# Kernel optimization log

Measured on AMD Instinct MI355X. Metric: run time of the kernel, lower is better.

## Reference

```python
import jax, jax.numpy as jnp
import numpy as np

H = 256


def _lstm_cell(inp, hx, cx, Wih, Whh, bih, bhh):
    # PyTorch LSTMCell: gate order i, f, g, o
    gates = inp @ Wih.T + bih + hx @ Whh.T + bhh
    i, f, g, o = jnp.split(gates, 4, axis=-1)
    c = jax.nn.sigmoid(f) * cx + jax.nn.sigmoid(i) * jnp.tanh(g)
    h = jax.nn.sigmoid(o) * jnp.tanh(c)
    return h, c


def _match(p_enc, q_enc, wq, wp, whr_w, whr_b, w_vec, w_b0, Wih, Whh, bih, bhh, reverse):
    # p_enc: (P,B,H) time-major passage; q_enc, wq: (Q,B,H); wp: (P,B,H)
    B = p_enc.shape[1]

    def step(carry, xs):
        hx, cx = carry
        wphp, p_t = xs                                  # (B,H), (B,H)
        wrhr = hx @ whr_w.T + whr_b                     # (B,H)
        g = jnp.tanh(wq + (wphp + wrhr))                # (Q,B,H)
        scores = jnp.einsum('qbh,h->bq', g, w_vec) + w_b0
        alpha = jax.nn.softmax(scores, axis=-1)         # (B,Q)
        attn = jnp.einsum('bq,qbh->bh', alpha, q_enc)   # (B,H)
        inp = jnp.concatenate([p_t, attn], axis=-1)     # (B,2H)
        hx, cx = _lstm_cell(inp, hx, cx, Wih, Whh, bih, bhh)
        return (hx, cx), hx

    init = (jnp.zeros((B, H), p_enc.dtype), jnp.zeros((B, H), p_enc.dtype))
    _, hs = jax.lax.scan(step, init, (wp, p_enc), reverse=reverse)
    return hs  # (P,B,H), always in natural time order


def setup_inputs() -> dict:
    key = jax.random.key(0)
    ks = jax.random.split(key, 20)
    s = 0.05
    return {
        'passage': jax.random.normal(ks[0], (64, 512, H), jnp.float32),
        'question': jax.random.normal(ks[1], (64, 64, H), jnp.float32),
        'whq_w': jax.random.normal(ks[2], (H, H), jnp.float32) * s,
        'whq_b': jax.random.normal(ks[3], (H,), jnp.float32) * s,
        'whp_w': jax.random.normal(ks[4], (H, H), jnp.float32) * s,
        'whp_b': jax.random.normal(ks[5], (H,), jnp.float32) * s,
        'whr_w': jax.random.normal(ks[6], (H, H), jnp.float32) * s,
        'whr_b': jax.random.normal(ks[7], (H,), jnp.float32) * s,
        'w_w': jax.random.normal(ks[8], (1, H), jnp.float32) * s,
        'w_b': jax.random.normal(ks[9], (1,), jnp.float32) * s,
        'fw_Wih': jax.random.normal(ks[10], (4 * H, 2 * H), jnp.float32) * s,
        'fw_Whh': jax.random.normal(ks[11], (4 * H, H), jnp.float32) * s,
        'fw_bih': jax.random.normal(ks[12], (4 * H,), jnp.float32) * s,
        'fw_bhh': jax.random.normal(ks[13], (4 * H,), jnp.float32) * s,
        'bw_Wih': jax.random.normal(ks[14], (4 * H, 2 * H), jnp.float32) * s,
        'bw_Whh': jax.random.normal(ks[15], (4 * H, H), jnp.float32) * s,
        'bw_bih': jax.random.normal(ks[16], (4 * H,), jnp.float32) * s,
        'bw_bhh': jax.random.normal(ks[17], (4 * H,), jnp.float32) * s,
    }


def reference(passage, question, whq_w, whq_b, whp_w, whp_b, whr_w, whr_b,
              w_w, w_b, fw_Wih, fw_Whh, fw_bih, fw_bhh,
              bw_Wih, bw_Whh, bw_bih, bw_bhh):
    p = jnp.swapaxes(passage, 0, 1)    # (P,B,H)
    q = jnp.swapaxes(question, 0, 1)   # (Q,B,H)
    wq = q @ whq_w.T + whq_b           # (Q,B,H)  (dropout p=0.0 -> identity)
    wp = p @ whp_w.T + whp_b           # (P,B,H)
    fw = _match(p, q, wq, wp, whr_w, whr_b, w_w[0], w_b[0],
                fw_Wih, fw_Whh, fw_bih, fw_bhh, reverse=False)
    bw = _match(p, q, wq, wp, whr_w, whr_b, w_w[0], w_b[0],
                bw_Wih, bw_Whh, bw_bih, bw_bhh, reverse=True)
    return jnp.concatenate([fw, bw], axis=-1)  # (P,B,2H)
```

## Files before the change

kernel.cpp:

```cpp
#include <hip/hip_runtime.h>

#define HN 256
#define QN 64
#define PN 512
#define CH 8

typedef float f4 __attribute__((ext_vector_type(4)));

__device__ __forceinline__ float dot4(f4 a, f4 b) {
  return a.x * b.x + a.y * b.y + a.z * b.z + a.w * b.w;
}
__device__ __forceinline__ float fast_sig(float x) {
  return __builtin_amdgcn_rcpf(1.f + __builtin_amdgcn_exp2f(-1.44269504f * x));
}
__device__ __forceinline__ float fast_tanh(float x) {
  return 1.f - 2.f * __builtin_amdgcn_rcpf(1.f + __builtin_amdgcn_exp2f(2.88539008f * x));
}

struct SMem {
  union {
    float q32[QN][HN];
    struct {
      alignas(16) float pgc[CH][1024];
      alignas(16) float wpc[CH][HN];
      alignas(16) float pch[CH][HN];
    } c;
  } u;
  alignas(16) float wqt[QN][HN + 4];
  alignas(16) float ww[HN];
  alignas(16) float hx[HN];
  float cx[HN];
  alignas(16) float wA[HN];
  float wrb[HN];
  float gates[1024];
  float scores[QN];
  alignas(16) float al[QN];
};
static_assert(sizeof(SMem) <= 160 * 1024, "LDS overflow");
static_assert(sizeof(SMem) > 80 * 1024, "want exactly 1 block/CU");

__global__ void __launch_bounds__(1024, 4)
match_kernel(const float* __restrict__ passage, const float* __restrict__ question,
             const float* __restrict__ whq_w, const float* __restrict__ whq_b,
             const float* __restrict__ whp_w, const float* __restrict__ whp_b,
             const float* __restrict__ whr_w, const float* __restrict__ whr_b,
             const float* __restrict__ w_w,
             const float* __restrict__ Wih_f, const float* __restrict__ Whh_f,
             const float* __restrict__ bih_f, const float* __restrict__ bhh_f,
             const float* __restrict__ Wih_b, const float* __restrict__ Whh_b,
             const float* __restrict__ bih_b, const float* __restrict__ bhh_b,
             float* __restrict__ out)
{
  __shared__ SMem sm;
  const int t = threadIdx.x;
  const int bid = blockIdx.x;
  const int e = bid & 7;
  const int dir = e >> 2;
  const int b = ((bid >> 3) << 2) | (e & 3);

  const float* Wih = dir ? Wih_b : Wih_f;
  const float* Whh = dir ? Whh_b : Whh_f;
  const float* bih = dir ? bih_b : bih_f;
  const float* bhh = dir ? bhh_b : bhh_f;

  const int qB = t >> 4;
  const int sg = t & 15;
  const int g2 = t >> 4;

  {
    const int q = t >> 4, c0 = (t & 15) * 16;
    const float* src = question + ((size_t)b * QN + q) * HN + c0;
    #pragma unroll
    for (int m = 0; m < 4; ++m)
      *(f4*)&sm.u.q32[q][c0 + 4 * m] = *(const f4*)(src + 4 * m);
  }
  if (t < HN) {
    sm.hx[t] = 0.f; sm.cx[t] = 0.f;
    sm.wrb[t] = whr_b[t]; sm.ww[t] = w_w[t];
  }
  __syncthreads();

  {
    const int h = t & 255, qh = (t >> 8) * 16;
    float acc[16];
    const float qb = whq_b[h];
    #pragma unroll
    for (int i2 = 0; i2 < 16; ++i2) acc[i2] = qb;
    const float* wrow = whq_w + (size_t)h * HN;
    for (int k = 0; k < HN; k += 4) {
      f4 w4 = *(const f4*)(wrow + k);
      #pragma unroll
      for (int i2 = 0; i2 < 16; ++i2) {
        f4 qv = *(const f4*)&sm.u.q32[qh + i2][k];
        acc[i2] += dot4(w4, qv);
      }
    }
    #pragma unroll
    for (int i2 = 0; i2 < 16; ++i2) sm.wqt[qh + i2][h] = acc[i2];
  }

  float gq[QN];
  #pragma unroll
  for (int q = 0; q < QN; ++q) gq[q] = 0.f;
  {
    const float* wrow = Wih + (size_t)t * 512 + 256;
    for (int i = 0; i < 64; ++i) {
      f4 w = *(const f4*)(wrow + 4 * i);
      #pragma unroll
      for (int q = 0; q < QN; ++q)
        gq[q] += dot4(w, *(const f4*)&sm.u.q32[q][4 * i]);
    }
  }
  const float biasr = bih[t] + bhh[t];
  __syncthreads();

  const int tb = dir ? (PN - 1) : 0;
  const int ts = dir ? -1 : 1;

  for (int s = 0; s < PN; ++s) {
    const int tau = s & (CH - 1);
    if (tau == 0) {
      if (t < 512) {
        const int tt = t >> 6, cc = (t & 63) * 4;
        const int trow = tb + ts * (s + tt);
        *(f4*)&sm.u.c.pch[tt][cc] =
            *(const f4*)(passage + ((size_t)b * PN + trow) * HN + cc);
      }
      __syncthreads();
      #pragma unroll
      for (int rr = 0; rr < 4; ++rr) {
        const int h = g2 + 64 * rr;
        const float* wrow = whp_w + (size_t)h * HN + sg * 4;
        float acc[CH];
        #pragma unroll
        for (int uu = 0; uu < CH; ++uu) acc[uu] = 0.f;
        #pragma unroll
        for (int m = 0; m < 4; ++m) {
          f4 w = *(const f4*)(wrow + m * 64);
          #pragma unroll
          for (int uu = 0; uu < CH; ++uu)
            acc[uu] += dot4(w, *(const f4*)&sm.u.c.pch[uu][m * 64 + sg * 4]);
        }
        #pragma unroll
        for (int uu = 0; uu < CH; ++uu) {
          acc[uu] += __shfl_xor(acc[uu], 1);
          acc[uu] += __shfl_xor(acc[uu], 2);
          acc[uu] += __shfl_xor(acc[uu], 4);
          acc[uu] += __shfl_xor(acc[uu], 8);
        }
        if (sg == rr) {
          const float pb = whp_b[h];
          #pragma unroll
          for (int uu = 0; uu < CH; ++uu) sm.u.c.wpc[uu][h] = acc[uu] + pb;
        }
      }
      #pragma unroll
      for (int rr = 0; rr < 16; ++rr) {
        const int r = g2 + 64 * rr;
        const float* wrow = Wih + (size_t)r * 512 + sg * 4;
        float acc[CH];
        #pragma unroll
        for (int uu = 0; uu < CH; ++uu) acc[uu] = 0.f;
        #pragma unroll
        for (int m = 0; m < 4; ++m) {
          f4 w = *(const f4*)(wrow + m * 64);
          #pragma unroll
          for (int uu = 0; uu < CH; ++uu)
            acc[uu] += dot4(w, *(const f4*)&sm.u.c.pch[uu][m * 64 + sg * 4]);
        }
        #pragma unroll
        for (int uu = 0; uu < CH; ++uu) {
          acc[uu] += __shfl_xor(acc[uu], 1);
          acc[uu] += __shfl_xor(acc[uu], 2);
          acc[uu] += __shfl_xor(acc[uu], 4);
          acc[uu] += __shfl_xor(acc[uu], 8);
        }
        if (sg == rr) {
          #pragma unroll
          for (int uu = 0; uu < CH; ++uu) sm.u.c.pgc[uu][r] = acc[uu];
        }
      }
      __syncthreads();
    }

    #pragma unroll
    for (int rr = 0; rr < 4; ++rr) {
      const int h = g2 + 64 * rr;
      const float* wrow = whr_w + (size_t)h * HN + sg * 4;
      float a = 0.f;
      #pragma unroll
      for (int m = 0; m < 4; ++m)
        a += dot4(*(const f4*)(wrow + m * 64),
                  *(const f4*)&sm.hx[m * 64 + sg * 4]);
      a += __shfl_xor(a, 1);
      a += __shfl_xor(a, 2);
      a += __shfl_xor(a, 4);
      a += __shfl_xor(a, 8);
      if (sg == rr) sm.wA[h] = a + sm.u.c.wpc[tau][h] + sm.wrb[h];
    }
    __syncthreads();

    {
      float sc = 0.f;
      #pragma unroll
      for (int jj = 0; jj < 4; ++jj) {
        f4 a4 = *(const f4*)&sm.wA[sg * 16 + 4 * jj];
        f4 q4 = *(const f4*)&sm.wqt[qB][sg * 16 + 4 * jj];
        f4 w4 = *(const f4*)&sm.ww[sg * 16 + 4 * jj];
        sc += fast_tanh(q4.x + a4.x) * w4.x;
        sc += fast_tanh(q4.y + a4.y) * w4.y;
        sc += fast_tanh(q4.z + a4.z) * w4.z;
        sc += fast_tanh(q4.w + a4.w) * w4.w;
      }
      sc += __shfl_xor(sc, 1);
      sc += __shfl_xor(sc, 2);
      sc += __shfl_xor(sc, 4);
      sc += __shfl_xor(sc, 8);
      if (sg == 0) sm.scores[qB] = sc;
    }
    __syncthreads();

    #pragma unroll
    for (int rr = 0; rr < 16; ++rr) {
      const int r = g2 + 64 * rr;
      const float* wrow = Whh + (size_t)r * HN + sg * 4;
      float a = 0.f;
      #pragma unroll
      for (int m = 0; m < 4; ++m)
        a += dot4(*(const f4*)(wrow + m * 64),
                  *(const f4*)&sm.hx[m * 64 + sg * 4]);
      a += __shfl_xor(a, 1);
      a += __shfl_xor(a, 2);
      a += __shfl_xor(a, 4);
      a += __shfl_xor(a, 8);
      if (sg == rr) sm.gates[r] = a;
    }
    if (t < 64) {
      float sv = sm.scores[t];
      float mx = sv;
      #pragma unroll
      for (int o = 1; o < 64; o <<= 1) mx = fmaxf(mx, __shfl_xor(mx, o));
      float ex = __builtin_amdgcn_exp2f(1.44269504f * (sv - mx));
      float sum = ex;
      #pragma unroll
      for (int o = 1; o < 64; o <<= 1) sum += __shfl_xor(sum, o);
      sm.al[t] = ex * __builtin_amdgcn_rcpf(sum);
    }
    __syncthreads();

    {
      float acc = sm.gates[t] + sm.u.c.pgc[tau][t] + biasr;
      #pragma unroll
      for (int jj = 0; jj < 16; ++jj) {
        f4 av = *(const f4*)&sm.al[4 * jj];
        acc += gq[4 * jj + 0] * av.x + gq[4 * jj + 1] * av.y
             + gq[4 * jj + 2] * av.z + gq[4 * jj + 3] * av.w;
      }
      sm.gates[t] = acc;
    }
    __syncthreads();

    if (t < HN) {
      float gi = sm.gates[t], gf = sm.gates[HN + t];
      float gg = sm.gates[2 * HN + t], go = sm.gates[3 * HN + t];
      float c = fast_sig(gf) * sm.cx[t] + fast_sig(gi) * fast_tanh(gg);
      float hn = fast_sig(go) * fast_tanh(c);
      sm.cx[t] = c;
      sm.hx[t] = hn;
      const int trow = tb + ts * s;
      out[((size_t)trow * 64 + b) * 512 + dir * HN + t] = hn;
    }
    __syncthreads();
  }
}

extern "C" void kernel_launch(void* const* d_in, const int* in_sizes, int n_in,
                              void* d_out, int out_size, void* d_ws, size_t ws_size,
                              hipStream_t stream) {
  (void)in_sizes; (void)n_in; (void)out_size; (void)d_ws; (void)ws_size;
  match_kernel<<<dim3(128), dim3(1024), 0, stream>>>(
      (const float*)d_in[0],
      (const float*)d_in[1],
      (const float*)d_in[2],
      (const float*)d_in[3],
      (const float*)d_in[4],
      (const float*)d_in[5],
      (const float*)d_in[6],
      (const float*)d_in[7],
      (const float*)d_in[8],
      (const float*)d_in[10],
      (const float*)d_in[11],
      (const float*)d_in[12],
      (const float*)d_in[13],
      (const float*)d_in[14],
      (const float*)d_in[15],
      (const float*)d_in[16],
      (const float*)d_in[17],
      (float*)d_out);
}
```

Measured before the change: 27.62 ms.

## Compute attention vector per step instead of precomputing Wih-projected question gates

The per-thread register array holding the input-weight projection of every question row (gq[64]) is removed. Each step now forms the attention vector alpha·q from global memory, then multiplies it by the attention half of Wih as an extra 1024x256 matvec with shuffle reductions. Alongside this, the LSTM biases are folded into the chunked passage-gate precompute, the chunk size is halved and the launch-bounds occupancy hint is dropped. The aim is to cut register pressure and the upfront precompute, but each sequential step now streams Wih and question data and pays an extra barrier.

```diff
diff --git a/kernel.cpp b/kernel.cpp
--- a/kernel.cpp
+++ b/kernel.cpp
@@ -3,7 +3,7 @@
 #define HN 256
 #define QN 64
 #define PN 512
-#define CH 8
+#define CH 4
 
 typedef float f4 __attribute__((ext_vector_type(4)));
 
@@ -28,10 +28,12 @@
   } u;
   alignas(16) float wqt[QN][HN + 4];
   alignas(16) float ww[HN];
+  float wrb[HN];
+  alignas(16) float biasg[1024];
   alignas(16) float hx[HN];
   float cx[HN];
   alignas(16) float wA[HN];
-  float wrb[HN];
+  alignas(16) float attn[HN];
   float gates[1024];
   float scores[QN];
   alignas(16) float al[QN];
@@ -39,7 +41,7 @@
 static_assert(sizeof(SMem) <= 160 * 1024, "LDS overflow");
 static_assert(sizeof(SMem) > 80 * 1024, "want exactly 1 block/CU");
 
-__global__ void __launch_bounds__(1024, 4)
+__global__ void __launch_bounds__(1024)
 match_kernel(const float* __restrict__ passage, const float* __restrict__ question,
              const float* __restrict__ whq_w, const float* __restrict__ whq_b,
              const float* __restrict__ whp_w, const float* __restrict__ whp_b,
@@ -78,6 +80,7 @@
     sm.hx[t] = 0.f; sm.cx[t] = 0.f;
     sm.wrb[t] = whr_b[t]; sm.ww[t] = w_w[t];
   }
+  sm.biasg[t] = bih[t] + bhh[t];
   __syncthreads();
 
   {
@@ -98,29 +101,16 @@
     #pragma unroll
     for (int i2 = 0; i2 < 16; ++i2) sm.wqt[qh + i2][h] = acc[i2];
   }
-
-  float gq[QN];
-  #pragma unroll
-  for (int q = 0; q < QN; ++q) gq[q] = 0.f;
-  {
-    const float* wrow = Wih + (size_t)t * 512 + 256;
-    for (int i = 0; i < 64; ++i) {
-      f4 w = *(const f4*)(wrow + 4 * i);
-      #pragma unroll
-      for (int q = 0; q < QN; ++q)
-        gq[q] += dot4(w, *(const f4*)&sm.u.q32[q][4 * i]);
-    }
-  }
-  const float biasr = bih[t] + bhh[t];
   __syncthreads();
 
   const int tb = dir ? (PN - 1) : 0;
   const int ts = dir ? -1 : 1;
+  const float* qglob = question + (size_t)b * QN * HN;
 
   for (int s = 0; s < PN; ++s) {
     const int tau = s & (CH - 1);
     if (tau == 0) {
-      if (t < 512) {
+      if (t < 256) {
         const int tt = t >> 6, cc = (t & 63) * 4;
         const int trow = tb + ts * (s + tt);
         *(f4*)&sm.u.c.pch[tt][cc] =
@@ -176,8 +166,9 @@
           acc[uu] += __shfl_xor(acc[uu], 8);
         }
         if (sg == rr) {
+          const float bg = sm.biasg[r];
           #pragma unroll
-          for (int uu = 0; uu < CH; ++uu) sm.u.c.pgc[uu][r] = acc[uu];
+          for (int uu = 0; uu < CH; ++uu) sm.u.c.pgc[uu][r] = acc[uu] + bg;
         }
       }
       __syncthreads();
@@ -248,15 +239,30 @@
     }
     __syncthreads();
 
-    {
-      float acc = sm.gates[t] + sm.u.c.pgc[tau][t] + biasr;
-      #pragma unroll
-      for (int jj = 0; jj < 16; ++jj) {
-        f4 av = *(const f4*)&sm.al[4 * jj];
-        acc += gq[4 * jj + 0] * av.x + gq[4 * jj + 1] * av.y
-             + gq[4 * jj + 2] * av.z + gq[4 * jj + 3] * av.w;
-      }
-      sm.gates[t] = acc;
+    if (t < HN) {
+      const float* qcol = qglob + t;
+      float a = 0.f;
+      #pragma unroll 16
+      for (int q = 0; q < QN; ++q)
+        a += sm.al[q] * qcol[(size_t)q * HN];
+      sm.attn[t] = a;
+    }
+    __syncthreads();
+
+    #pragma unroll
+    for (int rr = 0; rr < 16; ++rr) {
+      const int r = g2 + 64 * rr;
+      const float* wrow = Wih + (size_t)r * 512 + 256 + sg * 4;
+      float a = 0.f;
+      #pragma unroll
+      for (int m = 0; m < 4; ++m)
+        a += dot4(*(const f4*)(wrow + m * 64),
+                  *(const f4*)&sm.attn[m * 64 + sg * 4]);
+      a += __shfl_xor(a, 1);
+      a += __shfl_xor(a, 2);
+      a += __shfl_xor(a, 4);
+      a += __shfl_xor(a, 8);
+      if (sg == rr) sm.gates[r] += a + sm.u.c.pgc[tau][r];
     }
     __syncthreads();
 
```

Result: slower. 70.04 ms (+153.6%).
